# Kernel optimization log

Measured on AMD Instinct MI355X. Metric: run time of the kernel, lower is better.

## Reference

```python
import jax, jax.numpy as jnp
import numpy as np

B, S, V, E, H = 4096, 64, 100000, 128, 128

_PARAM_NAMES = ["Wz", "Uzl", "Uzr", "Wr", "Url", "Urr", "Wh", "Uhl", "Uhr"]


def setup_inputs() -> dict:
    key = jax.random.key(0)
    ks = jax.random.split(key, 2 + 2 * len(_PARAM_NAMES))
    inp = {"tokens": jax.random.randint(ks[0], (B, S), 0, V)}
    inp["emb"] = jax.random.normal(ks[1], (V, E), jnp.float32)
    i = 2
    for n in _PARAM_NAMES:
        din = E if n.startswith("W") else H
        inp[n] = jax.random.normal(ks[i], (din, H), jnp.float32) / np.sqrt(din).astype(np.float32)
        i += 1
        inp["b" + n] = jax.random.normal(ks[i], (H,), jnp.float32) * 0.01
        i += 1
    return inp


def _tree_gru(word, hl, hr, p):
    # word: [..., E], hl/hr: [..., H]
    z = jax.nn.sigmoid(word @ p["Wz"] + p["bWz"] + hl @ p["Uzl"] + p["bUzl"] + hr @ p["Uzr"] + p["bUzr"])
    r = jax.nn.sigmoid(word @ p["Wr"] + p["bWr"] + hl @ p["Url"] + p["bUrl"] + hr @ p["Urr"] + p["bUrr"])
    h_tilde = jnp.tanh(word @ p["Wh"] + p["bWh"] + (r * hl) @ p["Uhl"] + p["bUhl"] + (r * hr) @ p["Uhr"] + p["bUhr"])
    return z * hl + z * hr + (1.0 - z) * h_tilde


def reference(tokens, emb, Wz, bWz, Uzl, bUzl, Uzr, bUzr, Wr, bWr, Url, bUrl, Urr, bUrr, Wh, bWh, Uhl, bUhl, Uhr, bUhr):
    p = dict(Wz=Wz, bWz=bWz, Uzl=Uzl, bUzl=bUzl, Uzr=Uzr, bUzr=bUzr,
             Wr=Wr, bWr=bWr, Url=Url, bUrl=bUrl, Urr=Urr, bUrr=bUrr,
             Wh=Wh, bWh=bWh, Uhl=Uhl, bUhl=bUhl, Uhr=Uhr, bUhr=bUhr)
    x = emb[tokens]                                   # [B, S, E]
    h0 = jnp.zeros(x.shape[:2] + (H,), x.dtype)
    cur = _tree_gru(x, h0, h0, p)                     # leaf nodes [B, S, H]
    n = cur.shape[1]
    while n > 1:                                      # static loop over log2(S) tree levels
        left, right = cur[:, 0::2], cur[:, 1::2]      # pair adjacent nodes
        word0 = jnp.zeros(left.shape[:2] + (E,), cur.dtype)
        cur = _tree_gru(word0, left, right, p)
        n //= 2
    return cur.transpose(1, 0, 2)                     # [1, B, H] (matches torch transpose(0,1))
```

## Files before the change

kernel.cpp:

```cpp
#include <hip/hip_runtime.h>


typedef _Float16 half_t;
typedef __attribute__((ext_vector_type(2))) _Float16 f16x2;
typedef __attribute__((ext_vector_type(8))) _Float16 f16x8;
typedef __attribute__((ext_vector_type(4))) float f32x4;
typedef __attribute__((ext_vector_type(16))) float f32x16;

#define NTOK 262144
#define NB 4096
#define NV 100000

__device__ __forceinline__ float sigm(float x){
  float e = __expf(-x);
  return __builtin_amdgcn_rcpf(1.0f + e);
}
__device__ __forceinline__ float tanh_(float x){
  float e = __expf(2.f*x);
  float r = __builtin_amdgcn_rcpf(1.0f + e);
  return __builtin_fmaf(-2.0f, r, 1.0f);
}

__global__ void bias_k(const float* bWz,const float* bUzl,const float* bUzr,
                       const float* bWr,const float* bUrl,const float* bUrr,
                       const float* bWh,const float* bUhl,const float* bUhr, float* bc){
  int j = threadIdx.x;
  if (j < 128)      bc[j] = bWz[j]+bUzl[j]+bUzr[j];
  else if (j < 256){ int i=j-128; bc[j] = bWr[i]+bUrl[i]+bUrr[i]; }
  else if (j < 384){ int i=j-256; bc[j] = bWh[i]+bUhl[i]+bUhr[i]; }
}

__global__ __launch_bounds__(256) void wprep_k(
    const float* Wz, const float* Wh,
    const float* Uzl,const float* Uzr,const float* Url,const float* Urr,
    const float* Uhl,const float* Uhr, half_t* wb){
  int idx = blockIdx.x*256 + threadIdx.x;
  if (idx < 32768){
    const float* W = (idx < 16384) ? Wz : Wh;
    int t = idx & 16383;
    int w = t >> 11, ks = (t >> 9) & 3, l = (t >> 3) & 63, j = t & 7;
    int n = w*16 + (l & 15);
    int k = ks*32 + ((l >> 4) << 3) + j;
    wb[idx] = (half_t)W[k*128 + n];
  } else {
    int t = idx - 32768;
    int mat = t >> 15;
    t &= 32767;
    int cg = t >> 13, ks = (t >> 9) & 15, l = (t >> 3) & 63, j = t & 7;
    int n = cg*32 + (l & 31);
    int kp = ks*16 + ((l >> 5) << 3) + j;
    int k = kp >> 1;
    const float* U;
    if (mat == 0) U = (kp & 1) ? Uzr : Uzl;
    else if (mat == 1) U = (kp & 1) ? Urr : Url;
    else U = (kp & 1) ? Uhr : Uhl;
    wb[idx] = (half_t)U[k*128 + n];
  }
}

template<int MT>
__global__ __launch_bounds__(512, 8) void h1tab_k(
    const float* __restrict__ emb,
    const half_t* __restrict__ Wz_f, const half_t* __restrict__ Wh_f,
    const float* __restrict__ bc, half_t* __restrict__ t1)
{
  __shared__ __align__(16) _Float16 xs[MT*16][136];
  const int tid = threadIdx.x;
  const int m0  = blockIdx.x*(MT*16);
  #pragma unroll
  for (int it = 0; it < MT; it++){
    int idx = it*512 + tid;
    int m = idx >> 5, c = idx & 31;
    int row = m0 + m; if (row >= NV) row = 0;
    float4 v = ((const float4*)(emb + (size_t)row*128))[c];
    union { half_t h[4]; ushort4 u; } p;
    p.h[0]=(half_t)v.x; p.h[1]=(half_t)v.y; p.h[2]=(half_t)v.z; p.h[3]=(half_t)v.w;
    *(ushort4*)&xs[m][c*4] = p.u;
  }
  __syncthreads();
  const int w = tid>>6, l = tid&63;
  const int lr = l&15, lk = (l>>4)*8, lq = (l>>4)*4;
  const int col = w*16 + lr;

  f32x4 zacc[MT] = {}; f32x4 hacc[MT] = {};
  const half_t* wzp = Wz_f + ((w*4)*64 + l)*8;
  const half_t* whp = Wh_f + ((w*4)*64 + l)*8;
  f16x8 bz_n = *(const f16x8*)wzp;
  f16x8 bh_n = *(const f16x8*)whp;
  #pragma unroll
  for (int ks=0; ks<4; ks++){
    f16x8 bz = bz_n, bh = bh_n;
    if (ks < 3){
      bz_n = *(const f16x8*)(wzp + (ks+1)*512);
      bh_n = *(const f16x8*)(whp + (ks+1)*512);
    }
    #pragma unroll
    for (int mt=0; mt<MT; mt++){
      f16x8 a = *(const f16x8*)&xs[mt*16 + lr][ks*32 + lk];
      zacc[mt] = __builtin_amdgcn_mfma_f32_16x16x32_f16(a, bz, zacc[mt],0,0,0);
      hacc[mt] = __builtin_amdgcn_mfma_f32_16x16x32_f16(a, bh, hacc[mt],0,0,0);
    }
  }
  const float bzv = bc[col], bhv = bc[256+col];
  #pragma unroll
  for (int mt=0; mt<MT; mt++){
    #pragma unroll
    for (int q=0; q<4; q++){
      int row = m0 + mt*16 + lq + q;
      if (row < NV){
        float z  = sigm(zacc[mt][q] + bzv);
        float ht = tanh_(hacc[mt][q] + bhv);
        t1[(size_t)row*128 + col] = (half_t)((1.f-z)*ht);
      }
    }
  }
}

template<int MT, int WR, int GATHER>
__global__ __launch_bounds__(WR*256, 8) void tree_k(
    const half_t* __restrict__ hin, const int* __restrict__ tokens,
    half_t* __restrict__ hout, float* __restrict__ outf,
    const half_t* __restrict__ Uz_f, const half_t* __restrict__ Ur_f, const half_t* __restrict__ Uh_f,
    const float* __restrict__ bc, int last)
{
  constexpr int ROWS = WR*MT*32;
  constexpr int THREADS = WR*256;
  __shared__ __align__(16) _Float16 xs[ROWS][264];
  const int tid = threadIdx.x;
  const int m0  = blockIdx.x*ROWS;
  #pragma unroll
  for (int it = 0; it < MT*4; it++){
    int idx = it*THREADS + tid;
    int m = idx >> 5, c = idx & 31;
    const half_t *pl, *pr;
    if (GATHER){
      int tl = tokens[2*(m0+m)], tr = tokens[2*(m0+m)+1];
      pl = hin + (size_t)tl*128 + c*4;
      pr = hin + (size_t)tr*128 + c*4;
    } else {
      size_t base = (size_t)(2*(m0+m))*128 + c*4;
      pl = hin + base;
      pr = hin + base + 128;
    }
    uint2 A  = *(const uint2*)pl;
    uint2 Bv = *(const uint2*)pr;
    uint4 o;
    o.x = (A.x & 0xFFFFu) | (Bv.x << 16);
    o.y = (A.x >> 16)     | (Bv.x & 0xFFFF0000u);
    o.z = (A.y & 0xFFFFu) | (Bv.y << 16);
    o.w = (A.y >> 16)     | (Bv.y & 0xFFFF0000u);
    *(uint4*)&xs[m][c*8] = o;
  }
  __syncthreads();
  const int w = tid>>6, l = tid&63;
  const int cg = w & 3, rg = w >> 2;
  const int lc = l & 31, hi = l >> 5;
  const int lk8 = hi*8;
  const int col = cg*32 + lc;
  const int rowbase = rg*(MT*32);

  f32x16 zacc[MT] = {}; f32x16 racc[MT] = {};
  const half_t* uzp = Uz_f + ((cg*16)*64 + l)*8;
  const half_t* urp = Ur_f + ((cg*16)*64 + l)*8;
  f16x8 bz_n = *(const f16x8*)uzp;
  f16x8 br_n = *(const f16x8*)urp;
  #pragma unroll
  for (int ks=0; ks<16; ks++){
    f16x8 bz = bz_n, br = br_n;
    if (ks < 15){
      bz_n = *(const f16x8*)(uzp + (ks+1)*512);
      br_n = *(const f16x8*)(urp + (ks+1)*512);
    }
    #pragma unroll
    for (int mt=0; mt<MT; mt++){
      f16x8 a = *(const f16x8*)&xs[rowbase + mt*32 + lc][ks*16 + lk8];
      zacc[mt] = __builtin_amdgcn_mfma_f32_32x32x16_f16(a, bz, zacc[mt],0,0,0);
      racc[mt] = __builtin_amdgcn_mfma_f32_32x32x16_f16(a, br, racc[mt],0,0,0);
    }
  }
  __syncthreads();

  uint zp[MT][8], sp[MT][8];
  const float bzv = bc[col], brv = bc[128+col];
  #pragma unroll
  for (int mt=0; mt<MT; mt++){
    union { half_t h[16]; uint u[8]; } pz, ps;
    #pragma unroll
    for (int r=0; r<16; r++){
      int row = rowbase + mt*32 + (r&3) + 8*(r>>2) + 4*hi;
      union { uint u; f16x2 h2; } io;
      io.u = *(uint*)&xs[row][2*col];
      float z  = sigm(zacc[mt][r] + bzv);
      float rv = sigm(racc[mt][r] + brv);
      half_t rvh = (half_t)rv;
      f16x2 rv2; rv2[0]=rvh; rv2[1]=rvh;
      half_t sh = (half_t)(io.h2[0] + io.h2[1]);
      io.h2 = io.h2 * rv2;
      pz.h[r] = (half_t)z;
      ps.h[r] = sh;
      *(uint*)&xs[row][2*col] = io.u;
    }
    #pragma unroll
    for (int u8=0; u8<8; u8++){ zp[mt][u8]=pz.u[u8]; sp[mt][u8]=ps.u[u8]; }
  }
  __syncthreads();

  f32x16 ha[MT] = {};
  const half_t* uhp = Uh_f + ((cg*16)*64 + l)*8;
  f16x8 bh_n = *(const f16x8*)uhp;
  #pragma unroll
  for (int ks=0; ks<16; ks++){
    f16x8 bh = bh_n;
    if (ks < 15) bh_n = *(const f16x8*)(uhp + (ks+1)*512);
    #pragma unroll
    for (int mt=0; mt<MT; mt++){
      f16x8 a = *(const f16x8*)&xs[rowbase + mt*32 + lc][ks*16 + lk8];
      ha[mt] = __builtin_amdgcn_mfma_f32_32x32x16_f16(a, bh, ha[mt],0,0,0);
    }
  }
  const float bhv = bc[256+col];
  #pragma unroll
  for (int mt=0; mt<MT; mt++){
    union { half_t h[16]; uint u[8]; } pz, ps;
    #pragma unroll
    for (int u8=0; u8<8; u8++){ pz.u[u8]=zp[mt][u8]; ps.u[u8]=sp[mt][u8]; }
    #pragma unroll
    for (int r=0; r<16; r++){
      int row = rowbase + mt*32 + (r&3) + 8*(r>>2) + 4*hi;
      float ht = tanh_(ha[mt][r] + bhv);
      float z  = (float)pz.h[r];
      float s  = (float)ps.h[r];
      float o  = __builtin_fmaf(z, s - ht, ht);
      size_t off = (size_t)(m0+row)*128 + col;
      if (last) outf[off] = o;
      else      hout[off] = (half_t)o;
    }
  }
}

extern "C" void kernel_launch(void* const* d_in, const int* in_sizes, int n_in,
                              void* d_out, int out_size, void* d_ws, size_t ws_size,
                              hipStream_t stream) {
  const int*   tokens = (const int*)  d_in[0];
  const float* emb    = (const float*)d_in[1];
  const float* Wz  = (const float*)d_in[2];  const float* bWz  = (const float*)d_in[3];
  const float* Uzl = (const float*)d_in[4];  const float* bUzl = (const float*)d_in[5];
  const float* Uzr = (const float*)d_in[6];  const float* bUzr = (const float*)d_in[7];
  const float* Wr  = (const float*)d_in[8];  const float* bWr  = (const float*)d_in[9];
  const float* Url = (const float*)d_in[10]; const float* bUrl = (const float*)d_in[11];
  const float* Urr = (const float*)d_in[12]; const float* bUrr = (const float*)d_in[13];
  const float* Wh  = (const float*)d_in[14]; const float* bWh  = (const float*)d_in[15];
  const float* Uhl = (const float*)d_in[16]; const float* bUhl = (const float*)d_in[17];
  const float* Uhr = (const float*)d_in[18]; const float* bUhr = (const float*)d_in[19];

  float*  bc = (float*)d_ws;
  half_t* wb = (half_t*)((char*)d_ws + 4096);
  half_t* Wz_f = wb;
  half_t* Wh_f = wb + 16384;
  half_t* Uz_f = wb + 32768;
  half_t* Ur_f = wb + 65536;
  half_t* Uh_f = wb + 98304;
  half_t* t1 = (half_t*)((char*)d_ws + (1<<20));
  half_t* hA = t1 + (size_t)NV*128;
  half_t* hB = hA + (size_t)(NTOK/2)*128;

  bias_k<<<1, 384, 0, stream>>>(bWz,bUzl,bUzr,bWr,bUrl,bUrr,bWh,bUhl,bUhr, bc);
  wprep_k<<<512, 256, 0, stream>>>(Wz,Wh,Uzl,Uzr,Url,Urr,Uhl,Uhr, wb);

  h1tab_k<4><<<(NV + 63)/64, 512, 0, stream>>>(emb, Wz_f, Wh_f, bc, t1);

  float* outf = (float*)d_out;
  tree_k<1,1,1><<<4096, 256, 0, stream>>>(t1, tokens, hA, outf, Uz_f, Ur_f, Uh_f, bc, 0);
  tree_k<1,1,0><<<2048, 256, 0, stream>>>(hA, tokens, hB, outf, Uz_f, Ur_f, Uh_f, bc, 0);
  tree_k<1,1,0><<<1024, 256, 0, stream>>>(hB, tokens, hA, outf, Uz_f, Ur_f, Uh_f, bc, 0);
  tree_k<1,1,0><<<512,  256, 0, stream>>>(hA, tokens, hB, outf, Uz_f, Ur_f, Uh_f, bc, 0);
  tree_k<1,1,0><<<256,  256, 0, stream>>>(hB, tokens, hA, outf, Uz_f, Ur_f, Uh_f, bc, 0);
  tree_k<1,1,0><<<128,  256, 0, stream>>>(hA, tokens, hB, outf, Uz_f, Ur_f, Uh_f, bc, 1);
}
```

Baseline: 155.5 us.

## Give each wave its own 32-row tile in tree kernel, drop block barriers

The tree kernel now assigns each of the four waves an independent 32-row tile covering all 128 output columns, looping over the four column groups inside the wave. Before, the four waves split columns of one shared tile. Because waves no longer share LDS data, all __syncthreads are removed, and the grid shrinks by four. The manual weight prefetch in both kernels is replaced with direct loads. The cost is that each wave loads all weight columns, needs more registers for the per-column z/r values, and launches far fewer blocks at the small upper tree levels, leaving much of the GPU idle.

```diff
diff --git a/kernel.cpp b/kernel.cpp
--- a/kernel.cpp
+++ b/kernel.cpp
@@ -85,15 +85,10 @@
   f32x4 zacc[MT] = {}; f32x4 hacc[MT] = {};
   const half_t* wzp = Wz_f + ((w*4)*64 + l)*8;
   const half_t* whp = Wh_f + ((w*4)*64 + l)*8;
-  f16x8 bz_n = *(const f16x8*)wzp;
-  f16x8 bh_n = *(const f16x8*)whp;
   #pragma unroll
   for (int ks=0; ks<4; ks++){
-    f16x8 bz = bz_n, bh = bh_n;
-    if (ks < 3){
-      bz_n = *(const f16x8*)(wzp + (ks+1)*512);
-      bh_n = *(const f16x8*)(whp + (ks+1)*512);
-    }
+    f16x8 bz = *(const f16x8*)(wzp + ks*512);
+    f16x8 bh = *(const f16x8*)(whp + ks*512);
     #pragma unroll
     for (int mt=0; mt<MT; mt++){
       f16x8 a = *(const f16x8*)&xs[mt*16 + lr][ks*32 + lk];
@@ -116,21 +111,22 @@
   }
 }
 
-template<int MT, int WR, int GATHER>
-__global__ __launch_bounds__(WR*256, 8) void tree_k(
+template<int GATHER>
+__global__ __launch_bounds__(256) void tree_k(
     const half_t* __restrict__ hin, const int* __restrict__ tokens,
     half_t* __restrict__ hout, float* __restrict__ outf,
     const half_t* __restrict__ Uz_f, const half_t* __restrict__ Ur_f, const half_t* __restrict__ Uh_f,
     const float* __restrict__ bc, int last)
 {
-  constexpr int ROWS = WR*MT*32;
-  constexpr int THREADS = WR*256;
-  __shared__ __align__(16) _Float16 xs[ROWS][264];
+  __shared__ __align__(16) _Float16 xs[4][32][264];
   const int tid = threadIdx.x;
-  const int m0  = blockIdx.x*ROWS;
-  #pragma unroll
-  for (int it = 0; it < MT*4; it++){
-    int idx = it*THREADS + tid;
+  const int w = tid >> 6, l = tid & 63;
+  const int m0 = (blockIdx.x*4 + w) * 32;
+  _Float16 (*tile)[264] = xs[w];
+
+  #pragma unroll
+  for (int it = 0; it < 16; it++){
+    int idx = it*64 + l;
     int m = idx >> 5, c = idx & 31;
     const half_t *pl, *pr;
     if (GATHER){
@@ -149,91 +145,90 @@
     o.y = (A.x >> 16)     | (Bv.x & 0xFFFF0000u);
     o.z = (A.y & 0xFFFFu) | (Bv.y << 16);
     o.w = (A.y >> 16)     | (Bv.y & 0xFFFF0000u);
-    *(uint4*)&xs[m][c*8] = o;
-  }
-  __syncthreads();
-  const int w = tid>>6, l = tid&63;
-  const int cg = w & 3, rg = w >> 2;
+    *(uint4*)&tile[m][c*8] = o;
+  }
+
   const int lc = l & 31, hi = l >> 5;
   const int lk8 = hi*8;
-  const int col = cg*32 + lc;
-  const int rowbase = rg*(MT*32);
-
-  f32x16 zacc[MT] = {}; f32x16 racc[MT] = {};
-  const half_t* uzp = Uz_f + ((cg*16)*64 + l)*8;
-  const half_t* urp = Ur_f + ((cg*16)*64 + l)*8;
-  f16x8 bz_n = *(const f16x8*)uzp;
-  f16x8 br_n = *(const f16x8*)urp;
-  #pragma unroll
-  for (int ks=0; ks<16; ks++){
-    f16x8 bz = bz_n, br = br_n;
-    if (ks < 15){
-      bz_n = *(const f16x8*)(uzp + (ks+1)*512);
-      br_n = *(const f16x8*)(urp + (ks+1)*512);
-    }
-    #pragma unroll
-    for (int mt=0; mt<MT; mt++){
-      f16x8 a = *(const f16x8*)&xs[rowbase + mt*32 + lc][ks*16 + lk8];
-      zacc[mt] = __builtin_amdgcn_mfma_f32_32x32x16_f16(a, bz, zacc[mt],0,0,0);
-      racc[mt] = __builtin_amdgcn_mfma_f32_32x32x16_f16(a, br, racc[mt],0,0,0);
-    }
-  }
-  __syncthreads();
-
-  uint zp[MT][8], sp[MT][8];
-  const float bzv = bc[col], brv = bc[128+col];
-  #pragma unroll
-  for (int mt=0; mt<MT; mt++){
-    union { half_t h[16]; uint u[8]; } pz, ps;
-    #pragma unroll
-    for (int r=0; r<16; r++){
-      int row = rowbase + mt*32 + (r&3) + 8*(r>>2) + 4*hi;
-      union { uint u; f16x2 h2; } io;
-      io.u = *(uint*)&xs[row][2*col];
-      float z  = sigm(zacc[mt][r] + bzv);
-      float rv = sigm(racc[mt][r] + brv);
-      half_t rvh = (half_t)rv;
-      f16x2 rv2; rv2[0]=rvh; rv2[1]=rvh;
-      half_t sh = (half_t)(io.h2[0] + io.h2[1]);
-      io.h2 = io.h2 * rv2;
-      pz.h[r] = (half_t)z;
-      ps.h[r] = sh;
-      *(uint*)&xs[row][2*col] = io.u;
-    }
-    #pragma unroll
-    for (int u8=0; u8<8; u8++){ zp[mt][u8]=pz.u[u8]; sp[mt][u8]=ps.u[u8]; }
-  }
-  __syncthreads();
-
-  f32x16 ha[MT] = {};
-  const half_t* uhp = Uh_f + ((cg*16)*64 + l)*8;
-  f16x8 bh_n = *(const f16x8*)uhp;
-  #pragma unroll
-  for (int ks=0; ks<16; ks++){
-    f16x8 bh = bh_n;
-    if (ks < 15) bh_n = *(const f16x8*)(uhp + (ks+1)*512);
-    #pragma unroll
-    for (int mt=0; mt<MT; mt++){
-      f16x8 a = *(const f16x8*)&xs[rowbase + mt*32 + lc][ks*16 + lk8];
-      ha[mt] = __builtin_amdgcn_mfma_f32_32x32x16_f16(a, bh, ha[mt],0,0,0);
-    }
-  }
-  const float bhv = bc[256+col];
-  #pragma unroll
-  for (int mt=0; mt<MT; mt++){
-    union { half_t h[16]; uint u[8]; } pz, ps;
-    #pragma unroll
-    for (int u8=0; u8<8; u8++){ pz.u[u8]=zp[mt][u8]; ps.u[u8]=sp[mt][u8]; }
-    #pragma unroll
-    for (int r=0; r<16; r++){
-      int row = rowbase + mt*32 + (r&3) + 8*(r>>2) + 4*hi;
-      float ht = tanh_(ha[mt][r] + bhv);
-      float z  = (float)pz.h[r];
-      float s  = (float)ps.h[r];
-      float o  = __builtin_fmaf(z, s - ht, ht);
-      size_t off = (size_t)(m0+row)*128 + col;
-      if (last) outf[off] = o;
-      else      hout[off] = (half_t)o;
+
+  f16x2 zs[32], rv[32];
+  #pragma unroll
+  for (int cg = 0; cg < 4; cg++){
+    f32x16 zacc = {}; f32x16 racc = {};
+    const half_t* uzp = Uz_f + ((cg*16)*64 + l)*8;
+    const half_t* urp = Ur_f + ((cg*16)*64 + l)*8;
+    #pragma unroll
+    for (int ks=0; ks<16; ks++){
+      f16x8 bz = *(const f16x8*)(uzp + ks*512);
+      f16x8 br = *(const f16x8*)(urp + ks*512);
+      f16x8 a = *(const f16x8*)&tile[lc][ks*16 + lk8];
+      zacc = __builtin_amdgcn_mfma_f32_32x32x16_f16(a, bz, zacc,0,0,0);
+      racc = __builtin_amdgcn_mfma_f32_32x32x16_f16(a, br, racc,0,0,0);
+    }
+    const int col = cg*32 + lc;
+    const float bzv = bc[col], brv = bc[128+col];
+    #pragma unroll
+    for (int p = 0; p < 8; p++){
+      f16x2 zv2, rv2;
+      zv2[0] = (half_t)sigm(zacc[2*p]   + bzv);
+      zv2[1] = (half_t)sigm(zacc[2*p+1] + bzv);
+      rv2[0] = (half_t)sigm(racc[2*p]   + brv);
+      rv2[1] = (half_t)sigm(racc[2*p+1] + brv);
+      zs[cg*8+p] = zv2;
+      rv[cg*8+p] = rv2;
+    }
+  }
+
+  f16x2 sp[32];
+  #pragma unroll
+  for (int cg = 0; cg < 4; cg++){
+    const int col = cg*32 + lc;
+    #pragma unroll
+    for (int p = 0; p < 8; p++){
+      half_t s01[2];
+      #pragma unroll
+      for (int e = 0; e < 2; e++){
+        int r = 2*p + e;
+        int row = (r&3) + 8*(r>>2) + 4*hi;
+        union { uint u; f16x2 h2; } io;
+        io.u = *(uint*)&tile[row][2*col];
+        s01[e] = (half_t)(io.h2[0] + io.h2[1]);
+        half_t rvh = rv[cg*8+p][e];
+        f16x2 rv2; rv2[0]=rvh; rv2[1]=rvh;
+        io.h2 = io.h2 * rv2;
+        *(uint*)&tile[row][2*col] = io.u;
+      }
+      f16x2 sv; sv[0]=s01[0]; sv[1]=s01[1];
+      sp[cg*8+p] = sv;
+    }
+  }
+
+  #pragma unroll
+  for (int cg = 0; cg < 4; cg++){
+    f32x16 hacc = {};
+    const half_t* uhp = Uh_f + ((cg*16)*64 + l)*8;
+    #pragma unroll
+    for (int ks=0; ks<16; ks++){
+      f16x8 bh = *(const f16x8*)(uhp + ks*512);
+      f16x8 a = *(const f16x8*)&tile[lc][ks*16 + lk8];
+      hacc = __builtin_amdgcn_mfma_f32_32x32x16_f16(a, bh, hacc,0,0,0);
+    }
+    const int col = cg*32 + lc;
+    const float bhv = bc[256+col];
+    #pragma unroll
+    for (int p = 0; p < 8; p++){
+      #pragma unroll
+      for (int e = 0; e < 2; e++){
+        int r = 2*p + e;
+        int row = (r&3) + 8*(r>>2) + 4*hi;
+        float ht = tanh_(hacc[r] + bhv);
+        float z  = (float)zs[cg*8+p][e];
+        float s  = (float)sp[cg*8+p][e];
+        float o  = __builtin_fmaf(z, s - ht, ht);
+        size_t off = (size_t)(m0+row)*128 + col;
+        if (last) outf[off] = o;
+        else      hout[off] = (half_t)o;
+      }
     }
   }
 }
@@ -270,10 +265,10 @@
   h1tab_k<4><<<(NV + 63)/64, 512, 0, stream>>>(emb, Wz_f, Wh_f, bc, t1);
 
   float* outf = (float*)d_out;
-  tree_k<1,1,1><<<4096, 256, 0, stream>>>(t1, tokens, hA, outf, Uz_f, Ur_f, Uh_f, bc, 0);
-  tree_k<1,1,0><<<2048, 256, 0, stream>>>(hA, tokens, hB, outf, Uz_f, Ur_f, Uh_f, bc, 0);
-  tree_k<1,1,0><<<1024, 256, 0, stream>>>(hB, tokens, hA, outf, Uz_f, Ur_f, Uh_f, bc, 0);
-  tree_k<1,1,0><<<512,  256, 0, stream>>>(hA, tokens, hB, outf, Uz_f, Ur_f, Uh_f, bc, 0);
-  tree_k<1,1,0><<<256,  256, 0, stream>>>(hB, tokens, hA, outf, Uz_f, Ur_f, Uh_f, bc, 0);
-  tree_k<1,1,0><<<128,  256, 0, stream>>>(hA, tokens, hB, outf, Uz_f, Ur_f, Uh_f, bc, 1);
-}
+  tree_k<1><<<1024, 256, 0, stream>>>(t1, tokens, hA, outf, Uz_f, Ur_f, Uh_f, bc, 0);
+  tree_k<0><<<512,  256, 0, stream>>>(hA, tokens, hB, outf, Uz_f, Ur_f, Uh_f, bc, 0);
+  tree_k<0><<<256,  256, 0, stream>>>(hB, tokens, hA, outf, Uz_f, Ur_f, Uh_f, bc, 0);
+  tree_k<0><<<128,  256, 0, stream>>>(hA, tokens, hB, outf, Uz_f, Ur_f, Uh_f, bc, 0);
+  tree_k<0><<<64,   256, 0, stream>>>(hB, tokens, hA, outf, Uz_f, Ur_f, Uh_f, bc, 0);
+  tree_k<0><<<32,   256, 0, stream>>>(hA, tokens, hB, outf, Uz_f, Ur_f, Uh_f, bc, 1);
+}
```

Result: slower. 335.9 us (+116.0%).
